# Performance work log

Hardware: AMD Instinct MI355X
Metric: run time of the kernel (lower is better)

Reference implementation:

```python
import jax, jax.numpy as jnp
import numpy as np

N, D, N_CLASSES = 8192, 512, 128
POS_MARGIN = 1.0  # default path: sample_method=None, Dynamic_margin=None


def setup_inputs() -> dict:
    key = jax.random.key(0)
    k1, k2 = jax.random.split(key)
    x = jax.random.normal(k1, (N, D), dtype=jnp.float32)
    # metric-learning embeddings are L2-normalized so sim in [-1, 1]
    x = x / jnp.linalg.norm(x, axis=1, keepdims=True)
    targets = jax.random.randint(k2, (N,), 0, N_CLASSES, dtype=jnp.int64)
    return {"inputs": x, "targets": targets, "nonorm": 0}


def reference(inputs, targets, nonorm):
    n = inputs.shape[0]
    sim = jnp.matmul(inputs, inputs.T)                      # [n, n]
    same = targets[:, None] == targets[None, :]             # [n, n]
    pos_mask = same & (sim < POS_MARGIN)                    # drops self-sim == 1
    neg_mask = ~same

    # per-row masked log-sum-exp (sort in original is irrelevant to the sums)
    pos_sum = jnp.sum(jnp.where(pos_mask, jnp.exp(1.0 - sim), 0.0), axis=1)
    neg_sum = jnp.sum(jnp.where(neg_mask, jnp.exp(sim), 0.0), axis=1)
    pos_loss = jnp.log(pos_sum)
    neg_loss = jnp.log(neg_sum)

    has_neg = jnp.any(neg_mask, axis=1)                     # rows w/o negs are skipped
    loss = jnp.sum(jnp.where(has_neg, pos_loss + neg_loss, 0.0)) / n
    prec = jnp.mean(1.0 - has_neg.astype(jnp.float32))      # fraction of skipped rows

    # torch code reports means of the LAST row's pos/neg pairs
    last_pos = pos_mask[-1]
    last_neg = neg_mask[-1]
    mean_pos_sim = jnp.sum(jnp.where(last_pos, sim[-1], 0.0)) / jnp.sum(last_pos)
    mean_neg_sim = jnp.sum(jnp.where(last_neg, sim[-1], 0.0)) / jnp.sum(last_neg)
    return loss, prec, mean_pos_sim, mean_neg_sim
```

## Files before the change

kernel.cpp:

```cpp
#include <hip/hip_runtime.h>
#include <math.h>

#define N_ 8192
#define D_ 512
#define NC_ 128
#define T_ 64

typedef __attribute__((ext_vector_type(8))) short bf16x8;
typedef __attribute__((ext_vector_type(4))) float f32x4;
typedef __attribute__((ext_vector_type(4))) unsigned short us4;

static __device__ __forceinline__ unsigned short f2bf(float f) {
    union { float f; unsigned u; } c; c.f = f;
    unsigned u = c.u;
    u += 0x7fffu + ((u >> 16) & 1u);
    return (unsigned short)(u >> 16);
}

__global__ __launch_bounds__(256) void k_prep(const float* __restrict__ x,
                                              const int* __restrict__ tg,
                                              unsigned short* __restrict__ xb,
                                              double* __restrict__ sim_last,
                                              int* __restrict__ hist,
                                              int* __restrict__ done,
                                              int* __restrict__ skipAcc,
                                              double* __restrict__ lossAcc) {
    const int b = blockIdx.x;
    if (b < 4096) {
        int i = b * 256 + threadIdx.x;
        float4 v = reinterpret_cast<const float4*>(x)[i];
        us4 o = { f2bf(v.x), f2bf(v.y), f2bf(v.z), f2bf(v.w) };
        reinterpret_cast<us4*>(xb)[i] = o;
    } else if (b < 6144) {
        int j    = ((b - 4096) * 256 + threadIdx.x) >> 6;
        int lane = threadIdx.x & 63;
        const float* xl = x + (size_t)(N_ - 1) * D_;
        const float* xj = x + (size_t)j * D_;
        double acc = 0.0;
#pragma unroll
        for (int it = 0; it < 8; ++it) {
            int k = it * 64 + lane;
            acc += (double)xl[k] * (double)xj[k];
        }
#pragma unroll
        for (int m = 32; m >= 1; m >>= 1) acc += __shfl_xor(acc, m, 64);
        if (lane == 0) sim_last[j] = acc;
    } else {
        __shared__ int lh[NC_];
        if (threadIdx.x < NC_) lh[threadIdx.x] = 0;
        if (threadIdx.x == 0) { *done = 0; *skipAcc = 0; *lossAcc = 0.0; }
        __syncthreads();
        for (int i = threadIdx.x; i < N_; i += 256) atomicAdd(&lh[tg[i]], 1);
        __syncthreads();
        if (threadIdx.x < NC_) hist[threadIdx.x] = lh[threadIdx.x];
    }
}

__global__ __launch_bounds__(512, 4) void k_main(const unsigned short* __restrict__ xb,
                                                 const int* __restrict__ tg,
                                                 float* __restrict__ bufP,
                                                 float* __restrict__ bufN) {
    __shared__ alignas(16) unsigned short As[128 * 64];
    __shared__ alignas(16) unsigned short Bs[256 * 64];
    __shared__ int rowT[128];

    const int tid  = threadIdx.x;
    const int w    = tid >> 6;
    const int lane = tid & 63;
    const int q    = lane >> 4;
    const int l15  = lane & 15;
    const int wrow = w >> 2;
    const int wcol = w & 3;

    int rem = blockIdx.x;
    int it = 0;
    while (rem >= 32 - (it >> 1)) { rem -= 32 - (it >> 1); it++; }
    const int jt2  = (it >> 1) + rem;
    const int row0 = it * 128;
    const int col0 = jt2 * 256;

    const int bsub   = 2 * jt2 + (wcol >> 1);
    const bool rowOK = (bsub >= it);

    if (tid < 128) rowT[tid] = tg[row0 + tid];
    __syncthreads();

    int tR[4][4];
#pragma unroll
    for (int mi = 0; mi < 4; ++mi)
#pragma unroll
        for (int r = 0; r < 4; ++r)
            tR[mi][r] = rowT[wrow * 64 + mi * 16 + q * 4 + r];

    int tC[4];
#pragma unroll
    for (int ni = 0; ni < 4; ++ni)
        tC[ni] = tg[col0 + wcol * 64 + ni * 16 + l15];

    f32x4 acc[4][4];
#pragma unroll
    for (int mi = 0; mi < 4; ++mi)
#pragma unroll
        for (int ni = 0; ni < 4; ++ni)
            acc[mi][ni] = (f32x4){0.f, 0.f, 0.f, 0.f};

    for (int ks = 0; ks < 8; ++ks) {
        const int k0 = ks * 64;
        __syncthreads();
#pragma unroll
        for (int i2 = 0; i2 < 2; ++i2) {
            int slot = i2 * 512 + tid;
            int r  = slot >> 3;
            int s  = slot & 7;
            int g  = s ^ (r & 7);
            const unsigned short* ga = xb + (size_t)(row0 + r) * D_ + k0 + g * 8;
            __builtin_amdgcn_global_load_lds(
                (const __attribute__((address_space(1))) void*)ga,
                (__attribute__((address_space(3))) void*)(As + (i2 * 512 + w * 64) * 8),
                16, 0, 0);
        }
#pragma unroll
        for (int i2 = 0; i2 < 4; ++i2) {
            int slot = i2 * 512 + tid;
            int r  = slot >> 3;
            int s  = slot & 7;
            int g  = s ^ (r & 7);
            const unsigned short* gb = xb + (size_t)(col0 + r) * D_ + k0 + g * 8;
            __builtin_amdgcn_global_load_lds(
                (const __attribute__((address_space(1))) void*)gb,
                (__attribute__((address_space(3))) void*)(Bs + (i2 * 512 + w * 64) * 8),
                16, 0, 0);
        }
        __syncthreads();

#pragma unroll
        for (int kc = 0; kc < 2; ++kc) {
            bf16x8 aF[4], bF[4];
#pragma unroll
            for (int mi = 0; mi < 4; ++mi) {
                int rA = wrow * 64 + mi * 16 + l15;
                int g  = kc * 4 + q;
                int s  = g ^ (rA & 7);
                aF[mi] = *reinterpret_cast<const bf16x8*>(As + rA * 64 + s * 8);
            }
#pragma unroll
            for (int ni = 0; ni < 4; ++ni) {
                int rB = wcol * 64 + ni * 16 + l15;
                int g  = kc * 4 + q;
                int s  = g ^ (rB & 7);
                bF[ni] = *reinterpret_cast<const bf16x8*>(Bs + rB * 64 + s * 8);
            }
#pragma unroll
            for (int mi = 0; mi < 4; ++mi)
#pragma unroll
                for (int ni = 0; ni < 4; ++ni)
                    acc[mi][ni] = __builtin_amdgcn_mfma_f32_16x16x32_bf16(
                        aF[mi], bF[ni], acc[mi][ni], 0, 0, 0);
        }
    }

    float ps[4][4], ns[4][4];
    float cps[4], cns[4];
#pragma unroll
    for (int mi = 0; mi < 4; ++mi)
#pragma unroll
        for (int r = 0; r < 4; ++r) { ps[mi][r] = 0.f; ns[mi][r] = 0.f; }
#pragma unroll
    for (int ni = 0; ni < 4; ++ni) { cps[ni] = 0.f; cns[ni] = 0.f; }

    if (rowOK) {
#pragma unroll
        for (int mi = 0; mi < 4; ++mi)
#pragma unroll
            for (int ni = 0; ni < 4; ++ni)
#pragma unroll
                for (int r = 0; r < 4; ++r) {
                    float s = acc[mi][ni][r];
                    bool same = (tR[mi][r] == tC[ni]);
                    float e = __expf(same ? 1.0f - s : s);
                    float pe = (same && (s < 1.0f)) ? e : 0.0f;
                    float ne = same ? 0.0f : e;
                    ps[mi][r] += pe; ns[mi][r] += ne;
                    cps[ni]   += pe; cns[ni]   += ne;
                }
    }

    __syncthreads();
    float* scr = (float*)As;

#pragma unroll
    for (int mi = 0; mi < 4; ++mi)
#pragma unroll
        for (int r = 0; r < 4; ++r) {
            float p = ps[mi][r];
            float n = ns[mi][r];
#pragma unroll
            for (int m = 1; m < 16; m <<= 1) {
                p += __shfl_xor(p, m, 64);
                n += __shfl_xor(n, m, 64);
            }
            if (l15 == 0) {
                int rloc = wrow * 64 + mi * 16 + q * 4 + r;
                scr[wcol * 128 + rloc]       = p;
                scr[512 + wcol * 128 + rloc] = n;
            }
        }

#pragma unroll
    for (int ni = 0; ni < 4; ++ni) {
        float p = cps[ni];
        float n = cns[ni];
        p += __shfl_xor(p, 16, 64); p += __shfl_xor(p, 32, 64);
        n += __shfl_xor(n, 16, 64); n += __shfl_xor(n, 32, 64);
        if (q == 0) {
            int cloc = wcol * 64 + ni * 16 + l15;
            scr[1024 + wrow * 256 + cloc] = p;
            scr[1536 + wrow * 256 + cloc] = n;
        }
    }
    __syncthreads();

    if (tid < 128) {
        int r = tid;
        int s_row = it + jt2 - (it >> 1);
        size_t off = ((size_t)it * T_ + s_row) * 128 + r;
        bufP[off] = scr[r] + scr[128 + r] + scr[256 + r] + scr[384 + r];
        bufN[off] = scr[512 + r] + scr[640 + r] + scr[768 + r] + scr[896 + r];
    } else if (tid < 384) {
        int c  = tid - 128;
        int bc = 2 * jt2 + (c >> 7);
        if (bc > it) {
            size_t off = ((size_t)bc * T_ + it) * 128 + (c & 127);
            bufP[off] = scr[1024 + c] + scr[1280 + c];
            bufN[off] = scr[1536 + c] + scr[1792 + c];
        }
    }
}

__global__ __launch_bounds__(256) void k_tail(const float* __restrict__ bufP,
                                              const float* __restrict__ bufN,
                                              const int* __restrict__ tg,
                                              const int* __restrict__ hist,
                                              const double* __restrict__ sim_last,
                                              int* __restrict__ done,
                                              int* __restrict__ skipAcc,
                                              double* __restrict__ lossAcc,
                                              float* __restrict__ out) {
    __shared__ float  pn[256];
    __shared__ double sdA[256], sdB[256];
    __shared__ int    siA[256], siB[256];
    __shared__ int    amLast;

    const int tid  = threadIdx.x;
    const int t    = blockIdx.x;
    const int half = tid >> 7;
    const int r    = tid & 127;
    const int smax = t + 32 - (t >> 1);

    const float* buf  = half ? bufN : bufP;
    const float* base = buf + (size_t)t * T_ * 128 + r;
    float s = 0.f;
    for (int o = 0; o < smax; ++o) s += base[o * 128];
    pn[tid] = s;
    __syncthreads();

    double part = 0.0;
    int skip = 0;
    if (half == 0) {
        int gi = t * 128 + r;
        if (hist[tg[gi]] < N_) part = (double)(logf(pn[r]) + logf(pn[128 + r]));
        else skip = 1;
    }
    sdA[tid] = part; siA[tid] = skip;
    __syncthreads();
    for (int st = 128; st >= 1; st >>= 1) {
        if (tid < st) { sdA[tid] += sdA[tid + st]; siA[tid] += siA[tid + st]; }
        __syncthreads();
    }

    if (tid == 0) {
        atomicAdd(lossAcc, sdA[0]);
        atomicAdd(skipAcc, siA[0]);
        __threadfence();
        amLast = (atomicAdd(done, 1) == T_ - 1);
    }
    __syncthreads();
    if (!amLast) return;

    __shared__ double finLoss;
    __shared__ int    finSkip;
    if (tid == 0) {
        __threadfence();
        finLoss = atomicAdd(lossAcc, 0.0);
        finSkip = atomicAdd(skipAcc, 0);
    }

    double pd = 0.0, nd = 0.0;
    int pc = 0, nc = 0;
    int tlast = tg[N_ - 1];
    for (int j = tid; j < N_; j += 256) {
        double sv = sim_last[j];
        if (tg[j] == tlast) {
            if (sv < 1.0) { pd += sv; pc++; }
        } else {
            nd += sv; nc++;
        }
    }
    sdA[tid] = pd; sdB[tid] = nd; siA[tid] = pc; siB[tid] = nc;
    __syncthreads();
    for (int st = 128; st >= 1; st >>= 1) {
        if (tid < st) {
            sdA[tid] += sdA[tid + st]; sdB[tid] += sdB[tid + st];
            siA[tid] += siA[tid + st]; siB[tid] += siB[tid + st];
        }
        __syncthreads();
    }
    if (tid == 0) {
        out[0] = (float)(finLoss / (double)N_);
        out[1] = (float)finSkip / (float)N_;
        out[2] = (float)(sdA[0] / (double)siA[0]);
        out[3] = (float)(sdB[0] / (double)siB[0]);
    }
}

extern "C" void kernel_launch(void* const* d_in, const int* in_sizes, int n_in,
                              void* d_out, int out_size, void* d_ws, size_t ws_size,
                              hipStream_t stream) {
    const float* x  = (const float*)d_in[0];
    const int*   tg = (const int*)d_in[1];
    char* ws = (char*)d_ws;

    unsigned short* xb = (unsigned short*)ws;
    const size_t XB = (size_t)N_ * D_ * 2;
    double* sim_last = (double*)(ws + XB);
    float*  bufP     = (float*)(ws + XB + 65536);
    float*  bufN     = (float*)(ws + XB + 65536 + 2097152);
    char*   ctrl     = ws + XB + 65536 + 2 * 2097152;
    int*    hist     = (int*)ctrl;
    int*    done     = (int*)(ctrl + 512);
    int*    skipAcc  = (int*)(ctrl + 516);
    double* lossAcc  = (double*)(ctrl + 520);

    const int nblk = 1056;

    hipLaunchKernelGGL(k_prep, dim3(4096 + 2048 + 1), dim3(256), 0, stream,
                       x, tg, xb, sim_last, hist, done, skipAcc, lossAcc);
    hipLaunchKernelGGL(k_main, dim3(nblk), dim3(512), 0, stream, xb, tg, bufP, bufN);
    hipLaunchKernelGGL(k_tail, dim3(T_), dim3(256), 0, stream,
                       bufP, bufN, tg, hist, sim_last, done, skipAcc, lossAcc,
                       (float*)d_out);
}
```

Before: 173.1 us.

## Add producer warps with double-buffered LDS and flag-based sync in main GEMM

Splits the main kernel block into 8 consumer waves doing MFMA and 4 producer waves that stream A/B tiles into double-buffered LDS via global_load_lds. Block-wide barriers are replaced by shared-memory ready/done counters, so loads for the next K step can overlap compute on the current one. In exchange it doubles LDS use, raises block size to 768 with fewer blocks per CU, and adds spin-wait overhead. The producer waves' trailing __syncthreads calls must pair with barriers in the consumer path for the block to behave correctly.

Measured after the change: 186.9 us. +7.9%, slower.

```diff
diff --git a/kernel.cpp b/kernel.cpp
--- a/kernel.cpp
+++ b/kernel.cpp
@@ -56,21 +56,21 @@
     }
 }
 
-__global__ __launch_bounds__(512, 4) void k_main(const unsigned short* __restrict__ xb,
+__global__ __launch_bounds__(768, 3) void k_main(const unsigned short* __restrict__ xb,
                                                  const int* __restrict__ tg,
                                                  float* __restrict__ bufP,
                                                  float* __restrict__ bufN) {
-    __shared__ alignas(16) unsigned short As[128 * 64];
-    __shared__ alignas(16) unsigned short Bs[256 * 64];
+    __shared__ alignas(16) unsigned short As[2][1024 * 8];
+    __shared__ alignas(16) unsigned short Bs[2][2048 * 8];
     __shared__ int rowT[128];
+    __shared__ int ready[8];
+    __shared__ int doneC[8];
 
     const int tid  = threadIdx.x;
     const int w    = tid >> 6;
     const int lane = tid & 63;
     const int q    = lane >> 4;
     const int l15  = lane & 15;
-    const int wrow = w >> 2;
-    const int wcol = w & 3;
 
     int rem = blockIdx.x;
     int it = 0;
@@ -79,12 +79,57 @@
     const int row0 = it * 128;
     const int col0 = jt2 * 256;
 
+    if (tid < 128) rowT[tid] = tg[row0 + tid];
+    if (tid >= 128 && tid < 136) ready[tid - 128] = 0;
+    if (tid >= 136 && tid < 144) doneC[tid - 136] = 0;
+    __syncthreads();
+
+    if (w >= 8) {
+        const int pw = w - 8;
+        for (int s = 0; s < 8; ++s) {
+            if (s >= 2) {
+                while (__hip_atomic_load(&doneC[s - 2], __ATOMIC_ACQUIRE,
+                                         __HIP_MEMORY_SCOPE_WORKGROUP) < 8)
+                    __builtin_amdgcn_s_sleep(1);
+            }
+            const int k0 = s * 64;
+            unsigned short* Ad = As[s & 1];
+            unsigned short* Bd = Bs[s & 1];
+#pragma unroll
+            for (int i = 0; i < 4; ++i) {
+                int slot = i * 256 + pw * 64 + lane;
+                int r = slot >> 3, sl = slot & 7, g = sl ^ (r & 7);
+                const unsigned short* ga = xb + (size_t)(row0 + r) * D_ + k0 + g * 8;
+                __builtin_amdgcn_global_load_lds(
+                    (const __attribute__((address_space(1))) void*)ga,
+                    (__attribute__((address_space(3))) void*)(Ad + (i * 256 + pw * 64) * 8),
+                    16, 0, 0);
+            }
+#pragma unroll
+            for (int i = 0; i < 8; ++i) {
+                int slot = i * 256 + pw * 64 + lane;
+                int r = slot >> 3, sl = slot & 7, g = sl ^ (r & 7);
+                const unsigned short* gb = xb + (size_t)(col0 + r) * D_ + k0 + g * 8;
+                __builtin_amdgcn_global_load_lds(
+                    (const __attribute__((address_space(1))) void*)gb,
+                    (__attribute__((address_space(3))) void*)(Bd + (i * 256 + pw * 64) * 8),
+                    16, 0, 0);
+            }
+            __builtin_amdgcn_s_waitcnt(0x0F70);
+            if (lane == 0)
+                __hip_atomic_fetch_add(&ready[s], 1, __ATOMIC_RELEASE,
+                                       __HIP_MEMORY_SCOPE_WORKGROUP);
+        }
+        __syncthreads();
+        __syncthreads();
+        return;
+    }
+
+    const int wrow = w >> 2;
+    const int wcol = w & 3;
     const int bsub   = 2 * jt2 + (wcol >> 1);
     const bool rowOK = (bsub >= it);
 
-    if (tid < 128) rowT[tid] = tg[row0 + tid];
-    __syncthreads();
-
     int tR[4][4];
 #pragma unroll
     for (int mi = 0; mi < 4; ++mi)
@@ -104,35 +149,12 @@
         for (int ni = 0; ni < 4; ++ni)
             acc[mi][ni] = (f32x4){0.f, 0.f, 0.f, 0.f};
 
-    for (int ks = 0; ks < 8; ++ks) {
-        const int k0 = ks * 64;
-        __syncthreads();
-#pragma unroll
-        for (int i2 = 0; i2 < 2; ++i2) {
-            int slot = i2 * 512 + tid;
-            int r  = slot >> 3;
-            int s  = slot & 7;
-            int g  = s ^ (r & 7);
-            const unsigned short* ga = xb + (size_t)(row0 + r) * D_ + k0 + g * 8;
-            __builtin_amdgcn_global_load_lds(
-                (const __attribute__((address_space(1))) void*)ga,
-                (__attribute__((address_space(3))) void*)(As + (i2 * 512 + w * 64) * 8),
-                16, 0, 0);
-        }
-#pragma unroll
-        for (int i2 = 0; i2 < 4; ++i2) {
-            int slot = i2 * 512 + tid;
-            int r  = slot >> 3;
-            int s  = slot & 7;
-            int g  = s ^ (r & 7);
-            const unsigned short* gb = xb + (size_t)(col0 + r) * D_ + k0 + g * 8;
-            __builtin_amdgcn_global_load_lds(
-                (const __attribute__((address_space(1))) void*)gb,
-                (__attribute__((address_space(3))) void*)(Bs + (i2 * 512 + w * 64) * 8),
-                16, 0, 0);
-        }
-        __syncthreads();
-
+    for (int s = 0; s < 8; ++s) {
+        while (__hip_atomic_load(&ready[s], __ATOMIC_ACQUIRE,
+                                 __HIP_MEMORY_SCOPE_WORKGROUP) < 4)
+            __builtin_amdgcn_s_sleep(1);
+        const unsigned short* Ab = As[s & 1];
+        const unsigned short* Bb = Bs[s & 1];
 #pragma unroll
         for (int kc = 0; kc < 2; ++kc) {
             bf16x8 aF[4], bF[4];
@@ -140,15 +162,15 @@
             for (int mi = 0; mi < 4; ++mi) {
                 int rA = wrow * 64 + mi * 16 + l15;
                 int g  = kc * 4 + q;
-                int s  = g ^ (rA & 7);
-                aF[mi] = *reinterpret_cast<const bf16x8*>(As + rA * 64 + s * 8);
+                int sl = g ^ (rA & 7);
+                aF[mi] = *reinterpret_cast<const bf16x8*>(Ab + (rA * 8 + sl) * 8);
             }
 #pragma unroll
             for (int ni = 0; ni < 4; ++ni) {
                 int rB = wcol * 64 + ni * 16 + l15;
                 int g  = kc * 4 + q;
-                int s  = g ^ (rB & 7);
-                bF[ni] = *reinterpret_cast<const bf16x8*>(Bs + rB * 64 + s * 8);
+                int sl = g ^ (rB & 7);
+                bF[ni] = *reinterpret_cast<const bf16x8*>(Bb + (rB * 8 + sl) * 8);
             }
 #pragma unroll
             for (int mi = 0; mi < 4; ++mi)
@@ -157,6 +179,9 @@
                     acc[mi][ni] = __builtin_amdgcn_mfma_f32_16x16x32_bf16(
                         aF[mi], bF[ni], acc[mi][ni], 0, 0, 0);
         }
+        if (lane == 0)
+            __hip_atomic_fetch_add(&doneC[s], 1, __ATOMIC_RELEASE,
+                                   __HIP_MEMORY_SCOPE_WORKGROUP);
     }
 
     float ps[4][4], ns[4][4];
@@ -345,7 +370,7 @@
 
     hipLaunchKernelGGL(k_prep, dim3(4096 + 2048 + 1), dim3(256), 0, stream,
                        x, tg, xb, sim_last, hist, done, skipAcc, lossAcc);
-    hipLaunchKernelGGL(k_main, dim3(nblk), dim3(512), 0, stream, xb, tg, bufP, bufN);
+    hipLaunchKernelGGL(k_main, dim3(nblk), dim3(768), 0, stream, xb, tg, bufP, bufN);
     hipLaunchKernelGGL(k_tail, dim3(T_), dim3(256), 0, stream,
                        bufP, bufN, tg, hist, sim_last, done, skipAcc, lossAcc,
                        (float*)d_out);
```

## Load MFMA fragments directly from global memory, dropping LDS staging

Applied to the files above, without the earlier changes.

Replaces the LDS-staged tile loads (global_load_lds with swizzle and two barriers per k-step) with per-wave direct global loads of bf16x8 fragments into registers. The loads are double-buffered across 16 k-steps, and the GEMM is skipped entirely for waves whose sub-tile is below the diagonal (rowOK false). This removes LDS traffic and barriers and frees shared memory for occupancy. In exchange each wave re-reads A/B rows from global/L2 with no intra-block sharing, which raises memory traffic and register pressure. The launch_bounds occupancy hint is also dropped.

Measured after the change: 291.2 us. 68.2% more time.

```diff
diff --git a/kernel.cpp b/kernel.cpp
--- a/kernel.cpp
+++ b/kernel.cpp
@@ -56,13 +56,12 @@
     }
 }
 
-__global__ __launch_bounds__(512, 4) void k_main(const unsigned short* __restrict__ xb,
-                                                 const int* __restrict__ tg,
-                                                 float* __restrict__ bufP,
-                                                 float* __restrict__ bufN) {
-    __shared__ alignas(16) unsigned short As[128 * 64];
-    __shared__ alignas(16) unsigned short Bs[256 * 64];
+__global__ __launch_bounds__(512) void k_main(const unsigned short* __restrict__ xb,
+                                              const int* __restrict__ tg,
+                                              float* __restrict__ bufP,
+                                              float* __restrict__ bufN) {
     __shared__ int rowT[128];
+    __shared__ float scr[2048];
 
     const int tid  = threadIdx.x;
     const int w    = tid >> 6;
@@ -104,58 +103,38 @@
         for (int ni = 0; ni < 4; ++ni)
             acc[mi][ni] = (f32x4){0.f, 0.f, 0.f, 0.f};
 
-    for (int ks = 0; ks < 8; ++ks) {
-        const int k0 = ks * 64;
-        __syncthreads();
-#pragma unroll
-        for (int i2 = 0; i2 < 2; ++i2) {
-            int slot = i2 * 512 + tid;
-            int r  = slot >> 3;
-            int s  = slot & 7;
-            int g  = s ^ (r & 7);
-            const unsigned short* ga = xb + (size_t)(row0 + r) * D_ + k0 + g * 8;
-            __builtin_amdgcn_global_load_lds(
-                (const __attribute__((address_space(1))) void*)ga,
-                (__attribute__((address_space(3))) void*)(As + (i2 * 512 + w * 64) * 8),
-                16, 0, 0);
-        }
-#pragma unroll
-        for (int i2 = 0; i2 < 4; ++i2) {
-            int slot = i2 * 512 + tid;
-            int r  = slot >> 3;
-            int s  = slot & 7;
-            int g  = s ^ (r & 7);
-            const unsigned short* gb = xb + (size_t)(col0 + r) * D_ + k0 + g * 8;
-            __builtin_amdgcn_global_load_lds(
-                (const __attribute__((address_space(1))) void*)gb,
-                (__attribute__((address_space(3))) void*)(Bs + (i2 * 512 + w * 64) * 8),
-                16, 0, 0);
-        }
-        __syncthreads();
-
-#pragma unroll
-        for (int kc = 0; kc < 2; ++kc) {
-            bf16x8 aF[4], bF[4];
-#pragma unroll
-            for (int mi = 0; mi < 4; ++mi) {
-                int rA = wrow * 64 + mi * 16 + l15;
-                int g  = kc * 4 + q;
-                int s  = g ^ (rA & 7);
-                aF[mi] = *reinterpret_cast<const bf16x8*>(As + rA * 64 + s * 8);
-            }
-#pragma unroll
-            for (int ni = 0; ni < 4; ++ni) {
-                int rB = wcol * 64 + ni * 16 + l15;
-                int g  = kc * 4 + q;
-                int s  = g ^ (rB & 7);
-                bF[ni] = *reinterpret_cast<const bf16x8*>(Bs + rB * 64 + s * 8);
+    if (rowOK) {
+        const unsigned short* aB[4];
+        const unsigned short* bB[4];
+#pragma unroll
+        for (int mi = 0; mi < 4; ++mi)
+            aB[mi] = xb + (size_t)(row0 + wrow * 64 + mi * 16 + l15) * D_ + q * 8;
+#pragma unroll
+        for (int ni = 0; ni < 4; ++ni)
+            bB[ni] = xb + (size_t)(col0 + wcol * 64 + ni * 16 + l15) * D_ + q * 8;
+
+        bf16x8 aF[2][4], bF[2][4];
+#pragma unroll
+        for (int x4 = 0; x4 < 4; ++x4) {
+            aF[0][x4] = *reinterpret_cast<const bf16x8*>(aB[x4]);
+            bF[0][x4] = *reinterpret_cast<const bf16x8*>(bB[x4]);
+        }
+#pragma unroll
+        for (int t = 0; t < 16; ++t) {
+            const int cur = t & 1, nxt = cur ^ 1;
+            if (t < 15) {
+#pragma unroll
+                for (int x4 = 0; x4 < 4; ++x4) {
+                    aF[nxt][x4] = *reinterpret_cast<const bf16x8*>(aB[x4] + (t + 1) * 32);
+                    bF[nxt][x4] = *reinterpret_cast<const bf16x8*>(bB[x4] + (t + 1) * 32);
+                }
             }
 #pragma unroll
             for (int mi = 0; mi < 4; ++mi)
 #pragma unroll
                 for (int ni = 0; ni < 4; ++ni)
                     acc[mi][ni] = __builtin_amdgcn_mfma_f32_16x16x32_bf16(
-                        aF[mi], bF[ni], acc[mi][ni], 0, 0, 0);
+                        aF[cur][mi], bF[cur][ni], acc[mi][ni], 0, 0, 0);
         }
     }
 
@@ -184,9 +163,6 @@
                     cps[ni]   += pe; cns[ni]   += ne;
                 }
     }
-
-    __syncthreads();
-    float* scr = (float*)As;
 
 #pragma unroll
     for (int mi = 0; mi < 4; ++mi)
```
